# Performance work log

Hardware: AMD Instinct MI355X
Metric: run time of the kernel (lower is better)

The kernel has to match this reference:

```python
import jax, jax.numpy as jnp
import numpy as np

B, C, N, T = 16, 32, 1024, 128
R = 10  # low-rank bottleneck of W1/W2


def setup_inputs() -> dict:
    key = jax.random.key(0)
    k1, k2, k3, k4 = jax.random.split(key, 4)
    x = jax.random.normal(k1, (B, C, N, T), dtype=jnp.float32)
    W1 = jax.random.normal(k2, (R, N), dtype=jnp.float32) * 0.05
    W2 = jax.random.normal(k3, (R, N), dtype=jnp.float32) * 0.05
    alpha = jax.random.normal(k4, (C,), dtype=jnp.float32) * 0.1
    return {"x": x, "W1": W1, "W2": W2, "alpha": alpha}


def reference(x, W1, W2, alpha):
    # k = q = einsum('bint,i->btn', x, alpha): contract channels -> [B, T, N]
    k = jnp.einsum('bcnt,c->btn', x, alpha)
    # low-rank bilinear scores: (k @ W1^T) @ (k @ W2^T)^T -> [B, T, T]
    kw1 = jnp.einsum('btn,rn->btr', k, W1)   # [B, T, R]
    qw2 = jnp.einsum('btn,rn->btr', k, W2)   # [B, T, R]
    scores = jnp.einsum('btr,bsr->bts', kw1, qw2)  # [B, T, T]
    att = jax.nn.softmax(scores, axis=-1)
    # weighted sum over time: einsum('bti,bcni->bcnt', att, x)
    return jnp.einsum('bts,bcns->bcnt', att, x)
```

## Files before the change

kernel.cpp:

```cpp
#include <hip/hip_runtime.h>
#include <hip/hip_bf16.h>


#define B_ 16
#define C_ 32
#define N_ 1024
#define T_ 128
#define R_ 10
#define CH_ 16
#define NCH_ (N_ / CH_)

typedef __bf16 bf16x8 __attribute__((ext_vector_type(8)));
typedef __bf16 bf16x4 __attribute__((ext_vector_type(4)));
typedef float f32x4 __attribute__((ext_vector_type(4)));

__global__ __launch_bounds__(256) void k_reduce_c(const float* __restrict__ x,
                                                  const float* __restrict__ alpha,
                                                  float* __restrict__ k) {
    int bid = blockIdx.x;
    int b   = bid >> 7;
    int nc  = bid & 127;
    int tid = threadIdx.x;
    int nl  = tid >> 5;
    int lc  = tid & 31;
    int n   = nc * 8 + nl;
    const float4* xb = reinterpret_cast<const float4*>(
        x + ((size_t)(b * C_) * N_ + n) * T_) + lc;
    float4 acc = {0.f, 0.f, 0.f, 0.f};
    #pragma unroll 8
    for (int c = 0; c < C_; ++c) {
        float a = alpha[c];
        float4 v = xb[(size_t)c * (N_ * T_ / 4)];
        acc.x += a * v.x; acc.y += a * v.y; acc.z += a * v.z; acc.w += a * v.w;
    }
    reinterpret_cast<float4*>(k + ((size_t)b * N_ + n) * T_)[lc] = acc;
}

__global__ __launch_bounds__(128) void kw_partial(const float* __restrict__ k,
                                                  const float* __restrict__ W1,
                                                  const float* __restrict__ W2,
                                                  float* __restrict__ p1,
                                                  float* __restrict__ p2) {
    __shared__ __align__(16) float ws[NCH_][20];
    int bid = blockIdx.x;
    int b   = bid >> 4;
    int ch  = bid & (CH_ - 1);
    int n0  = ch * NCH_;
    int t   = threadIdx.x;
    for (int i = t; i < NCH_ * R_; i += 128) {
        int r = i / NCH_, nl = i % NCH_;
        ws[nl][r]      = W1[r * N_ + n0 + nl];
        ws[nl][R_ + r] = W2[r * N_ + n0 + nl];
    }
    __syncthreads();
    float a1[R_] = {}, a2[R_] = {};
    const float* kb = k + ((size_t)b * N_ + n0) * T_ + t;
    for (int nl = 0; nl < NCH_; ++nl) {
        float kv = kb[nl * T_];
        float wv[20];
        const float4* wr = reinterpret_cast<const float4*>(&ws[nl][0]);
        #pragma unroll
        for (int q = 0; q < 5; ++q) *reinterpret_cast<float4*>(&wv[q * 4]) = wr[q];
        #pragma unroll
        for (int r = 0; r < R_; ++r) {
            a1[r] += kv * wv[r];
            a2[r] += kv * wv[R_ + r];
        }
    }
    size_t o = ((size_t)(b * CH_ + ch) * T_ + t) * R_;
    #pragma unroll
    for (int r = 0; r < R_; ++r) { p1[o + r] = a1[r]; p2[o + r] = a2[r]; }
}

__global__ __launch_bounds__(128) void scores_softmax(const float* __restrict__ p1,
                                                      const float* __restrict__ p2,
                                                      __bf16* __restrict__ att) {
    __shared__ __align__(16) float kw1s[T_][12];
    __shared__ __align__(16) float kw2s[T_][12];
    __shared__ float sc[T_][T_ + 1];
    int b = blockIdx.x;
    int t = threadIdx.x;
    #pragma unroll
    for (int r = 0; r < R_; ++r) {
        float s1 = 0.f, s2 = 0.f;
        for (int ch = 0; ch < CH_; ++ch) {
            size_t o = ((size_t)(b * CH_ + ch) * T_ + t) * R_ + r;
            s1 += p1[o]; s2 += p2[o];
        }
        kw1s[t][r] = s1; kw2s[t][r] = s2;
    }
    __syncthreads();
    float myw[R_];
    #pragma unroll
    for (int r = 0; r < R_; ++r) myw[r] = kw1s[t][r];
    float mx = -1e30f;
    for (int s = 0; s < T_; ++s) {
        float wv[12];
        const float4* qr = reinterpret_cast<const float4*>(&kw2s[s][0]);
        #pragma unroll
        for (int q = 0; q < 3; ++q) *reinterpret_cast<float4*>(&wv[q * 4]) = qr[q];
        float v = 0.f;
        #pragma unroll
        for (int r = 0; r < R_; ++r) v += myw[r] * wv[r];
        sc[t][s] = v;
        mx = fmaxf(mx, v);
    }
    float sum = 0.f;
    for (int s = 0; s < T_; ++s) {
        float e = __expf(sc[t][s] - mx);
        sc[t][s] = e;
        sum += e;
    }
    float inv = 1.0f / sum;
    for (int s = 0; s < T_; ++s) sc[t][s] *= inv;
    __syncthreads();
    for (int i = 0; i < T_; ++i)
        att[((size_t)b * T_ + i) * T_ + t] = (__bf16)sc[i][t];
}

__global__ __launch_bounds__(256) void out_gemm(const float* __restrict__ x,
                                                const __bf16* __restrict__ att,
                                                float* __restrict__ out) {
    __shared__ __align__(16) __bf16 attl[T_][136];
    __shared__ __align__(16) __bf16 xsl[64][136];
    int bid = blockIdx.x;
    int nc  = bid & 15;
    int c   = (bid >> 4) & 31;
    int b   = bid >> 9;
    int tid = threadIdx.x;
    size_t slab = ((size_t)(b * C_ + c) * N_ + nc * 64) * T_;

    const uint4* ga = reinterpret_cast<const uint4*>(att + (size_t)b * T_ * T_);
    #pragma unroll
    for (int i = 0; i < 8; ++i) {
        int e = i * 256 + tid;
        int el = e * 8;
        *reinterpret_cast<uint4*>(&attl[el >> 7][el & 127]) = ga[e];
    }
    const float4* gx = reinterpret_cast<const float4*>(x + slab);
    #pragma unroll
    for (int i = 0; i < 8; ++i) {
        int e = i * 256 + tid;
        int el = e * 4;
        float4 v = gx[e];
        bf16x4 h = {(__bf16)v.x, (__bf16)v.y, (__bf16)v.z, (__bf16)v.w};
        *reinterpret_cast<bf16x4*>(&xsl[el >> 7][el & 127]) = h;
    }
    __syncthreads();

    int w = tid >> 6, lane = tid & 63;
    int r16 = lane & 15, g = lane >> 4;
    f32x4 acc[8] = {};
    #pragma unroll
    for (int ks = 0; ks < 4; ++ks) {
        bf16x8 af = *reinterpret_cast<const bf16x8*>(&xsl[w * 16 + r16][ks * 32 + g * 8]);
        #pragma unroll
        for (int tt = 0; tt < 8; ++tt) {
            bf16x8 bfr = *reinterpret_cast<const bf16x8*>(&attl[tt * 16 + r16][ks * 32 + g * 8]);
            acc[tt] = __builtin_amdgcn_mfma_f32_16x16x32_bf16(af, bfr, acc[tt], 0, 0, 0);
        }
    }
    float* o = out + slab;
    #pragma unroll
    for (int tt = 0; tt < 8; ++tt) {
        #pragma unroll
        for (int j = 0; j < 4; ++j)
            o[(size_t)(w * 16 + g * 4 + j) * T_ + tt * 16 + r16] = acc[tt][j];
    }
}

extern "C" void kernel_launch(void* const* d_in, const int* in_sizes, int n_in,
                              void* d_out, int out_size, void* d_ws, size_t ws_size,
                              hipStream_t stream) {
    const float* x     = (const float*)d_in[0];
    const float* W1    = (const float*)d_in[1];
    const float* W2    = (const float*)d_in[2];
    const float* alpha = (const float*)d_in[3];
    float* out = (float*)d_out;

    float* k  = (float*)d_ws;
    float* p1 = k + (size_t)B_ * N_ * T_;
    float* p2 = p1 + (size_t)B_ * CH_ * T_ * R_;
    __bf16* att = (__bf16*)(p2 + (size_t)B_ * CH_ * T_ * R_);

    k_reduce_c<<<dim3(B_ * (N_ / 8)), dim3(256), 0, stream>>>(x, alpha, k);
    kw_partial<<<dim3(B_ * CH_), dim3(128), 0, stream>>>(k, W1, W2, p1, p2);
    scores_softmax<<<dim3(B_), dim3(128), 0, stream>>>(p1, p2, att);
    out_gemm<<<dim3(B_ * C_ * (N_ / 64)), dim3(256), 0, stream>>>(x, att, out);
}
```

Measured before the change: 190.4 us.

## Swizzle LDS tiles, retile MFMA waves, and vectorize output and attention stores

The output GEMM drops the padded LDS arrays in favour of an XOR-swizzled 256-byte row layout, which keeps reads conflict-free without padding. Each wave now computes a 64x32 tile, and the operand roles are swapped (attention as A, x as B) so every lane holds four consecutive t values and can write the output with 16-byte f32x4 stores instead of scalar strided stores. The softmax kernel also writes each attention row directly as packed bf16x8 vectors, which removes the transpose pass through shared memory and the second barrier. The swizzle index arithmetic has to line up exactly between the store and load sides, and if it does not the results are wrong.

Result: no change. 190.4 us (+0.0%).

```diff
diff --git a/kernel.cpp b/kernel.cpp
--- a/kernel.cpp
+++ b/kernel.cpp
@@ -112,60 +112,84 @@
         sum += e;
     }
     float inv = 1.0f / sum;
-    for (int s = 0; s < T_; ++s) sc[t][s] *= inv;
-    __syncthreads();
-    for (int i = 0; i < T_; ++i)
-        att[((size_t)b * T_ + i) * T_ + t] = (__bf16)sc[i][t];
+    __bf16* arow = att + ((size_t)b * T_ + t) * T_;
+    for (int s8 = 0; s8 < T_; s8 += 8) {
+        bf16x8 h;
+        #pragma unroll
+        for (int q = 0; q < 8; ++q) h[q] = (__bf16)(sc[t][s8 + q] * inv);
+        *reinterpret_cast<bf16x8*>(arow + s8) = h;
+    }
 }
 
 __global__ __launch_bounds__(256) void out_gemm(const float* __restrict__ x,
                                                 const __bf16* __restrict__ att,
                                                 float* __restrict__ out) {
-    __shared__ __align__(16) __bf16 attl[T_][136];
-    __shared__ __align__(16) __bf16 xsl[64][136];
+    __shared__ __align__(16) __bf16 attl[T_][T_];
+    __shared__ __align__(16) __bf16 xsl[64][T_];
     int bid = blockIdx.x;
     int nc  = bid & 15;
     int c   = (bid >> 4) & 31;
     int b   = bid >> 9;
     int tid = threadIdx.x;
     size_t slab = ((size_t)(b * C_ + c) * N_ + nc * 64) * T_;
+    char* attb = reinterpret_cast<char*>(&attl[0][0]);
+    char* xb   = reinterpret_cast<char*>(&xsl[0][0]);
 
     const uint4* ga = reinterpret_cast<const uint4*>(att + (size_t)b * T_ * T_);
     #pragma unroll
     for (int i = 0; i < 8; ++i) {
-        int e = i * 256 + tid;
-        int el = e * 8;
-        *reinterpret_cast<uint4*>(&attl[el >> 7][el & 127]) = ga[e];
+        int e   = i * 256 + tid;
+        int row = e >> 4;
+        int bc  = ((e & 15) * 16) ^ ((row & 7) << 4);
+        *reinterpret_cast<uint4*>(attb + row * 256 + bc) = ga[e];
     }
     const float4* gx = reinterpret_cast<const float4*>(x + slab);
     #pragma unroll
     for (int i = 0; i < 8; ++i) {
-        int e = i * 256 + tid;
-        int el = e * 4;
+        int e   = i * 256 + tid;
+        int row = e >> 5;
         float4 v = gx[e];
         bf16x4 h = {(__bf16)v.x, (__bf16)v.y, (__bf16)v.z, (__bf16)v.w};
-        *reinterpret_cast<bf16x4*>(&xsl[el >> 7][el & 127]) = h;
+        int bc = ((e & 31) * 8) ^ ((row & 7) << 4);
+        *reinterpret_cast<bf16x4*>(xb + row * 256 + bc) = h;
     }
     __syncthreads();
 
-    int w = tid >> 6, lane = tid & 63;
+    int wave = tid >> 6, lane = tid & 63;
     int r16 = lane & 15, g = lane >> 4;
-    f32x4 acc[8] = {};
+    int wt = wave & 1, wn = wave >> 1;
+    int swz = (r16 & 7) << 4;
+    f32x4 acc[2][4] = {};
     #pragma unroll
     for (int ks = 0; ks < 4; ++ks) {
-        bf16x8 af = *reinterpret_cast<const bf16x8*>(&xsl[w * 16 + r16][ks * 32 + g * 8]);
-        #pragma unroll
-        for (int tt = 0; tt < 8; ++tt) {
-            bf16x8 bfr = *reinterpret_cast<const bf16x8*>(&attl[tt * 16 + r16][ks * 32 + g * 8]);
-            acc[tt] = __builtin_amdgcn_mfma_f32_16x16x32_bf16(af, bfr, acc[tt], 0, 0, 0);
-        }
+        int kc = ks * 64 + g * 16;
+        bf16x8 a[4], bx[2];
+        #pragma unroll
+        for (int tt = 0; tt < 4; ++tt) {
+            int row = wt * 64 + tt * 16 + r16;
+            a[tt] = *reinterpret_cast<const bf16x8*>(attb + row * 256 + (kc ^ swz));
+        }
+        #pragma unroll
+        for (int nn = 0; nn < 2; ++nn) {
+            int row = wn * 32 + nn * 16 + r16;
+            bx[nn] = *reinterpret_cast<const bf16x8*>(xb + row * 256 + (kc ^ swz));
+        }
+        #pragma unroll
+        for (int nn = 0; nn < 2; ++nn)
+            #pragma unroll
+            for (int tt = 0; tt < 4; ++tt)
+                acc[nn][tt] = __builtin_amdgcn_mfma_f32_16x16x32_bf16(
+                    a[tt], bx[nn], acc[nn][tt], 0, 0, 0);
     }
     float* o = out + slab;
     #pragma unroll
-    for (int tt = 0; tt < 8; ++tt) {
-        #pragma unroll
-        for (int j = 0; j < 4; ++j)
-            o[(size_t)(w * 16 + g * 4 + j) * T_ + tt * 16 + r16] = acc[tt][j];
+    for (int nn = 0; nn < 2; ++nn) {
+        int n_l = wn * 32 + nn * 16 + r16;
+        #pragma unroll
+        for (int tt = 0; tt < 4; ++tt) {
+            int t_l = wt * 64 + tt * 16 + g * 4;
+            *reinterpret_cast<f32x4*>(o + (size_t)n_l * T_ + t_l) = acc[nn][tt];
+        }
     }
 }
 
```
